# Kernel optimization log

Measured on AMD Instinct MI355X. Metric: run time of the kernel, lower is better.

## Reference

```python
import jax, jax.numpy as jnp
import numpy as np

C = 128
N = 4096
B = 4
NEG = -9e15


def _bn(x, g, b):
    # training-mode BatchNorm1d over (batch, N); x: [B, C, N]
    mean = x.mean(axis=(0, 2), keepdims=True)
    var = x.var(axis=(0, 2), keepdims=True)  # biased, like torch BN
    xh = (x - mean) * jax.lax.rsqrt(var + 1e-5)
    return xh * g[None, :, None] + b[None, :, None]


def _sa(x, mask2, wqk, wv, bv, wt, bt, g, b):
    # x: [B, C, N]; wqk: [C//4, C] (q and k share weights)
    xq = jnp.einsum('oc,bcn->bno', wqk, x)          # [B, N, C/4]
    xk = jnp.einsum('oc,bcm->bom', wqk, x)          # [B, C/4, N]
    energy = jnp.einsum('bno,bom->bnm', xq, xk)     # [B, N, N]
    energy = jnp.where(mask2, energy, NEG)
    attn = jax.nn.softmax(energy, axis=-1)
    # offset-attention: column-wise L1 renormalization
    attn = attn / (1e-9 + attn.sum(axis=1, keepdims=True))
    xv = jnp.einsum('oc,bcn->bon', wv, x) + bv[None, :, None]
    x_r = jnp.einsum('bcn,bnm->bcm', xv, attn)      # [B, C, N]
    x_r = jax.nn.relu(_bn(jnp.einsum('oc,bcn->bon', wt, x - x_r) + bt[None, :, None], g, b))
    return x + x_r


def setup_inputs() -> dict:
    key = jax.random.key(0)
    ks = jax.random.split(key, 12)
    s = 1.0 / np.sqrt(C)
    return {
        'x': jax.random.normal(ks[0], (B, C, N), jnp.float32),
        'mask': jax.random.randint(ks[1], (B, N), 0, 2, jnp.int32),
        'w1': jax.random.normal(ks[2], (C, C), jnp.float32) * s,
        'g1': jnp.ones((C,), jnp.float32),
        'b1': jnp.zeros((C,), jnp.float32),
        'w2': jax.random.normal(ks[3], (C, C), jnp.float32) * s,
        'g2': jnp.ones((C,), jnp.float32),
        'b2': jnp.zeros((C,), jnp.float32),
        'wqk': jax.random.normal(ks[4], (4, C // 4, C), jnp.float32) * s,
        'wv': jax.random.normal(ks[5], (4, C, C), jnp.float32) * s,
        'bv': jax.random.normal(ks[6], (4, C), jnp.float32) * 0.01,
        'wt': jax.random.normal(ks[7], (4, C, C), jnp.float32) * s,
        'bt': jax.random.normal(ks[8], (4, C), jnp.float32) * 0.01,
        'sg': jnp.ones((4, C), jnp.float32),
        'sb': jnp.zeros((4, C), jnp.float32),
    }


def reference(x, mask, w1, g1, b1, w2, g2, b2, wqk, wv, bv, wt, bt, sg, sb):
    m = mask.astype(bool)
    mask2 = m[:, :, None] & m[:, None, :]           # [B, N, N]
    x = jax.nn.relu(_bn(jnp.einsum('oc,bcn->bon', w1, x), g1, b1))
    x = jax.nn.relu(_bn(jnp.einsum('oc,bcn->bon', w2, x), g2, b2))
    outs = []
    h = x
    for i in range(4):
        h = _sa(h, mask2, wqk[i], wv[i], bv[i], wt[i], bt[i], sg[i], sb[i])
        outs.append(h)
    return jnp.concatenate(outs, axis=1)            # [B, 4C, N]
```

## Files before the change

### kernel.cpp

```cpp
#include <hip/hip_runtime.h>
#include <hip/hip_fp16.h>

constexpr int C = 128;
constexpr int N = 4096;
constexpr int B = 4;

typedef _Float16 f16x8 __attribute__((ext_vector_type(8)));
typedef _Float16 f16x4 __attribute__((ext_vector_type(4)));
typedef float    f32x4 __attribute__((ext_vector_type(4)));

__global__ __launch_bounds__(256) void k_wcvt(const float* __restrict__ w1,
                                              const float* __restrict__ w2,
                                              const float* __restrict__ wv,
                                              const float* __restrict__ wt,
                                              const float* __restrict__ wqk,
                                              _Float16* __restrict__ WF) {
  const int g = blockIdx.x * 256 + threadIdx.x;
  const float* src; int off;
  if (g < 4096)       { src = w1;  off = g; }
  else if (g < 8192)  { src = w2;  off = g - 4096; }
  else if (g < 24576) { src = wv;  off = g - 8192; }
  else if (g < 40960) { src = wt;  off = g - 24576; }
  else                { src = wqk; off = g - 40960; }
  const float4 v = ((const float4*)src)[off];
  f16x4 h = {(_Float16)v.x, (_Float16)v.y, (_Float16)v.z, (_Float16)v.w};
  *(f16x4*)&WF[(size_t)g * 4] = h;
}

__global__ __launch_bounds__(1024) void k_mask(const int* __restrict__ mask,
                                               int* __restrict__ psum,
                                               int* __restrict__ nvb) {
  const int b = blockIdx.x, tid = threadIdx.x;
  __shared__ int wsum[16];
  const int4 mv = *(const int4*)&mask[b * N + tid * 4];
  const int m0 = (mv.x != 0), m1 = (mv.y != 0), m2 = (mv.z != 0), m3 = (mv.w != 0);
  const int s0 = m0, s1 = s0 + m1, s2 = s1 + m2, s3 = s2 + m3;
  const int lane = tid & 63, w = tid >> 6;
  int sc = s3;
#pragma unroll
  for (int o = 1; o < 64; o <<= 1) {
    const int v = __shfl_up(sc, o, 64);
    if (lane >= o) sc += v;
  }
  if (lane == 63) wsum[w] = sc;
  __syncthreads();
  if (tid < 16) {
    int v = wsum[tid];
#pragma unroll
    for (int o = 1; o < 16; o <<= 1) {
      const int u = __shfl_up(v, o, 64);
      if (tid >= o) v += u;
    }
    wsum[tid] = v;
  }
  __syncthreads();
  const int excl = ((w > 0) ? wsum[w - 1] : 0) + sc - s3;
  int4 pv;
  pv.x = excl; pv.y = excl + s0; pv.z = excl + s1; pv.w = excl + s2;
  *(int4*)&psum[b * N + tid * 4] = pv;
  if (tid == 0) nvb[b] = wsum[15];
}

template<bool BIAS, bool STAT>
__global__ __launch_bounds__(512) void k_gwm(const _Float16* __restrict__ WF,
                                             const float* __restrict__ X,
                                             const float* __restrict__ bias,
                                             float* __restrict__ Y,
                                             float* __restrict__ bnpart) {
  __shared__ _Float16 XT[64 * 136];
  __shared__ float statP[4][64], statQ[4][64];
  const int tid = threadIdx.x;
  const int n0 = blockIdx.x * 64, oh = blockIdx.y, b = blockIdx.z;
  const float* Xb = X + (size_t)(b * C) * N + n0;
#pragma unroll
  for (int i = 0; i < 4; i++) {
    const int idx = tid + i * 512;
    const int c = idx >> 4, q = idx & 15;
    const float4 v = *(const float4*)&Xb[(size_t)c * N + q * 4];
    XT[(q * 4 + 0) * 136 + c] = (_Float16)v.x;
    XT[(q * 4 + 1) * 136 + c] = (_Float16)v.y;
    XT[(q * 4 + 2) * 136 + c] = (_Float16)v.z;
    XT[(q * 4 + 3) * 136 + c] = (_Float16)v.w;
  }
  __syncthreads();
  const int w = tid >> 6, lane = tid & 63, quad = lane >> 4, lr = lane & 15;
  const int nt = w & 3, og = w >> 2;
  const int ob[2] = {oh * 64 + og * 16, oh * 64 + (og + 2) * 16};
  f16x8 aW[2][4];
#pragma unroll
  for (int t = 0; t < 2; t++)
#pragma unroll
    for (int kc = 0; kc < 4; kc++)
      aW[t][kc] = *(const f16x8*)&WF[(size_t)(ob[t] + lr) * 128 + kc * 32 + quad * 8];
  f32x4 acc[2];
  acc[0] = (f32x4){0.f, 0.f, 0.f, 0.f};
  acc[1] = (f32x4){0.f, 0.f, 0.f, 0.f};
#pragma unroll
  for (int kc = 0; kc < 4; kc++) {
    const f16x8 bf = *(const f16x8*)&XT[(nt * 16 + lr) * 136 + kc * 32 + quad * 8];
    acc[0] = __builtin_amdgcn_mfma_f32_16x16x32_f16(aW[0][kc], bf, acc[0], 0, 0, 0);
    acc[1] = __builtin_amdgcn_mfma_f32_16x16x32_f16(aW[1][kc], bf, acc[1], 0, 0, 0);
  }
#pragma unroll
  for (int t = 0; t < 2; t++) {
#pragma unroll
    for (int r = 0; r < 4; r++) {
      const int o = ob[t] + quad * 4 + r;
      const float val = acc[t][r] + (BIAS ? bias[o] : 0.f);
      Y[(size_t)(b * C + o) * N + n0 + nt * 16 + lr] = val;
      if (STAT) {
        float s = val, q = val * val;
        s += __shfl_xor(s, 1, 64); q += __shfl_xor(q, 1, 64);
        s += __shfl_xor(s, 2, 64); q += __shfl_xor(q, 2, 64);
        s += __shfl_xor(s, 4, 64); q += __shfl_xor(q, 4, 64);
        s += __shfl_xor(s, 8, 64); q += __shfl_xor(q, 8, 64);
        if (lr == 0) { statP[nt][o - oh * 64] = s; statQ[nt][o - oh * 64] = q; }
      }
    }
  }
  if (STAT) {
    __syncthreads();
    if (tid < 64) {
      const int o = oh * 64 + tid;
      const float s = statP[0][tid] + statP[1][tid] + statP[2][tid] + statP[3][tid];
      const float q = statQ[0][tid] + statQ[1][tid] + statQ[2][tid] + statQ[3][tid];
      const int part = blockIdx.x * 4 + b;
      bnpart[o * 512 + part] = s;
      bnpart[o * 512 + 256 + part] = q;
    }
  }
}

__global__ __launch_bounds__(256) void k_qv(const _Float16* __restrict__ WFv,
                                            const _Float16* __restrict__ WFqk,
                                            const float* __restrict__ X,
                                            const float* __restrict__ bv,
                                            const int* __restrict__ mask,
                                            const int* __restrict__ psum,
                                            _Float16* __restrict__ XVc,
                                            _Float16* __restrict__ QT,
                                            _Float16* __restrict__ QTc,
                                            float* __restrict__ xvp) {
  __shared__ _Float16 XT[32 * 136];
  __shared__ float SP[2][128];
  const int tid = threadIdx.x;
  const int n0 = blockIdx.x * 32, b = blockIdx.y;
  const float* Xb = X + (size_t)(b * C) * N + n0;
#pragma unroll
  for (int i = 0; i < 4; i++) {
    const int idx = tid + i * 256;
    const int c = idx >> 3, q = idx & 7;
    const float4 v = *(const float4*)&Xb[(size_t)c * N + q * 4];
    XT[(q * 4 + 0) * 136 + c] = (_Float16)v.x;
    XT[(q * 4 + 1) * 136 + c] = (_Float16)v.y;
    XT[(q * 4 + 2) * 136 + c] = (_Float16)v.z;
    XT[(q * 4 + 3) * 136 + c] = (_Float16)v.w;
  }
  __syncthreads();
  const int w = tid >> 6, lane = tid & 63, quad = lane >> 4, lr = lane & 15;
  const int nt = w & 1, og = w >> 1;
  const int n = n0 + nt * 16 + lr;
  const int vld = mask[b * N + n] != 0;
  const int jc = psum[b * N + n];
  f32x4 acc[5];
  const _Float16* Aptr[5];
  int otl[5];
#pragma unroll
  for (int j = 0; j < 5; j++) {
    acc[j] = (f32x4){0.f, 0.f, 0.f, 0.f};
    const int ot = og + 2 * j;
    otl[j] = ot;
    Aptr[j] = (ot < 8) ? (WFv + (size_t)(ot * 16 + lr) * 128)
                       : (WFqk + (size_t)((ot - 8) * 16 + lr) * 128);
  }
#pragma unroll
  for (int kc = 0; kc < 4; kc++) {
    const f16x8 bf = *(const f16x8*)&XT[(nt * 16 + lr) * 136 + kc * 32 + quad * 8];
#pragma unroll
    for (int j = 0; j < 5; j++) {
      const f16x8 a = *(const f16x8*)&Aptr[j][kc * 32 + quad * 8];
      acc[j] = __builtin_amdgcn_mfma_f32_16x16x32_f16(a, bf, acc[j], 0, 0, 0);
    }
  }
#pragma unroll
  for (int j = 0; j < 5; j++) {
    const int ot = otl[j];
    if (ot < 8) {
      float v[4];
#pragma unroll
      for (int r = 0; r < 4; r++) v[r] = acc[j][r] + bv[ot * 16 + quad * 4 + r];
      if (vld) {
#pragma unroll
        for (int r = 0; r < 4; r++)
          XVc[(size_t)(b * C + ot * 16 + quad * 4 + r) * N + jc] = (_Float16)v[r];
      }
      float s[4];
#pragma unroll
      for (int r = 0; r < 4; r++) s[r] = vld ? 0.f : v[r];
#pragma unroll
      for (int o = 1; o <= 8; o <<= 1) {
#pragma unroll
        for (int r = 0; r < 4; r++) s[r] += __shfl_xor(s[r], o, 64);
      }
      if (lr == 0) {
#pragma unroll
        for (int r = 0; r < 4; r++) SP[nt][ot * 16 + quad * 4 + r] = s[r];
      }
    } else {
      f16x4 qv;
#pragma unroll
      for (int r = 0; r < 4; r++) qv[r] = (_Float16)acc[j][r];
      const int qo = (ot - 8) * 16 + quad * 4;
      *(f16x4*)&QT[((size_t)b * N + n) * 32 + qo] = qv;
      if (vld) *(f16x4*)&QTc[((size_t)b * N + jc) * 32 + qo] = qv;
    }
  }
  __syncthreads();
  if (tid < 128)
    xvp[(size_t)(b * C + tid) * 128 + blockIdx.x] = SP[0][tid] + SP[1][tid];
}

__global__ __launch_bounds__(64) void k_xvr(const float* __restrict__ xvp,
                                            float* __restrict__ xvi) {
  const int c = blockIdx.x, b = blockIdx.y, tid = threadIdx.x;
  const float* src = xvp + (size_t)(b * C + c) * 128;
  float v = src[tid] + src[tid + 64];
#pragma unroll
  for (int o = 1; o <= 32; o <<= 1) v += __shfl_xor(v, o, 64);
  if (tid == 0) xvi[b * C + c] = v;
}

__global__ __launch_bounds__(512) void k_sm(const _Float16* __restrict__ QTc,
                                            const int* __restrict__ nvb,
                                            float* __restrict__ rowmax,
                                            float* __restrict__ rowsi) {
  const int b = blockIdx.y;
  const int Nv = nvb[b];
  const int NvpB = (Nv + 63) & ~63;
  const int n0 = blockIdx.x * 64;
  if (n0 >= NvpB) return;
  __shared__ float mb[N];
  __shared__ float red[2][64];
  __shared__ float rmS[64];
  const int tid = threadIdx.x;
  const _Float16* Qb = QTc + (size_t)b * N * 32;
#pragma unroll
  for (int i = 0; i < 8; i++) {
    const int v = tid + i * 512;
    mb[v] = (v < Nv) ? 0.0f : -1e30f;
  }
  const int w = tid >> 6, lane = tid & 63, quad = lane >> 4, lr = lane & 15;
  const int nw = (w & 3) * 16, mh = (w >> 2) * 64;
  const f16x8 aF = *(const f16x8*)&Qb[(size_t)(n0 + nw + lr) * 32 + quad * 8];
  __syncthreads();
  float mx[4] = {-3e38f, -3e38f, -3e38f, -3e38f};
  for (int ms = 0; ms < NvpB; ms += 128) {
#pragma unroll
    for (int t = 0; t < 4; t++) {
      const int mrow = ms + mh + t * 16 + lr;
      const f16x8 bF = *(const f16x8*)&Qb[(size_t)mrow * 32 + quad * 8];
      f32x4 d = (f32x4){0.f, 0.f, 0.f, 0.f};
      d = __builtin_amdgcn_mfma_f32_16x16x32_f16(aF, bF, d, 0, 0, 0);
      const float bias = mb[mrow];
#pragma unroll
      for (int r = 0; r < 4; r++) mx[r] = fmaxf(mx[r], d[r] + bias);
    }
  }
#pragma unroll
  for (int r = 0; r < 4; r++) {
    float v = mx[r];
    v = fmaxf(v, __shfl_xor(v, 1, 64));
    v = fmaxf(v, __shfl_xor(v, 2, 64));
    v = fmaxf(v, __shfl_xor(v, 4, 64));
    v = fmaxf(v, __shfl_xor(v, 8, 64));
    mx[r] = v;
  }
  if (lr == 0)
#pragma unroll
    for (int r = 0; r < 4; r++) red[w >> 2][nw + quad * 4 + r] = mx[r];
  __syncthreads();
  if (tid < 64) rmS[tid] = fmaxf(red[0][tid], red[1][tid]);
  __syncthreads();
  float rmr[4];
#pragma unroll
  for (int r = 0; r < 4; r++) rmr[r] = rmS[nw + quad * 4 + r];
  float s[4] = {0.f, 0.f, 0.f, 0.f};
  for (int ms = 0; ms < NvpB; ms += 128) {
#pragma unroll
    for (int t = 0; t < 4; t++) {
      const int mrow = ms + mh + t * 16 + lr;
      const f16x8 bF = *(const f16x8*)&Qb[(size_t)mrow * 32 + quad * 8];
      f32x4 d = (f32x4){0.f, 0.f, 0.f, 0.f};
      d = __builtin_amdgcn_mfma_f32_16x16x32_f16(aF, bF, d, 0, 0, 0);
      const float bias = mb[mrow];
#pragma unroll
      for (int r = 0; r < 4; r++) s[r] += __expf(d[r] + bias - rmr[r]);
    }
  }
#pragma unroll
  for (int r = 0; r < 4; r++) {
    float v = s[r];
    v += __shfl_xor(v, 1, 64);
    v += __shfl_xor(v, 2, 64);
    v += __shfl_xor(v, 4, 64);
    v += __shfl_xor(v, 8, 64);
    s[r] = v;
  }
  __syncthreads();
  if (lr == 0)
#pragma unroll
    for (int r = 0; r < 4; r++) red[w >> 2][nw + quad * 4 + r] = s[r];
  __syncthreads();
  if (tid < 64) {
    const int row = n0 + tid;
    const float tot = red[0][tid] + red[1][tid];
    const bool valid = row < Nv;
    rowmax[b * N + row] = valid ? rmS[tid] : 1e30f;
    rowsi[b * N + row] = valid ? (1.0f / tot) : 0.0f;
  }
}

__global__ __launch_bounds__(512, 4) void k_pv(const _Float16* __restrict__ QT,
                                               const _Float16* __restrict__ QTc,
                                               const _Float16* __restrict__ XVc,
                                               const float* __restrict__ H,
                                               const int* __restrict__ mask,
                                               const float* __restrict__ rowmax,
                                               const float* __restrict__ rowsi,
                                               const int* __restrict__ nvb,
                                               const float* __restrict__ xvi,
                                               float* __restrict__ Td) {
  __shared__ _Float16 XVs[2][128 * 72];
  __shared__ _Float16 Ps[2][32 * 72];
  __shared__ float colPart[4][32];
  __shared__ float colS[32];
  const int tid = threadIdx.x;
  const int m0 = blockIdx.x * 32, b = blockIdx.y;
  const int Nv = nvb[b];
  const int ns = ((Nv + 63) & ~63) >> 6;
  const _Float16* Qa = QT + (size_t)b * N * 32;
  const _Float16* Qc = QTc + (size_t)b * N * 32;
  const _Float16* XVb = XVc + (size_t)(b * C) * N;
  const float* rmB = rowmax + b * N;
  const float* riB = rowsi + b * N;
  const int w = tid >> 6, lane = tid & 63, quad = lane >> 4, lr = lane & 15;
  const int msub = w & 1, nsub = w >> 1;
  const f16x8 aG = *(const f16x8*)&Qa[(size_t)(m0 + msub * 16 + lr) * 32 + quad * 8];
  float vmb[4];
#pragma unroll
  for (int r = 0; r < 4; r++)
    vmb[r] = (mask[b * N + m0 + msub * 16 + quad * 4 + r] != 0) ? 0.0f : -1e30f;
  const int sc0 = tid >> 3, sh0 = tid & 7;
  const int sc1 = sc0 + 64;
  f32x4 acc[2];
  acc[0] = (f32x4){0.f, 0.f, 0.f, 0.f};
  acc[1] = (f32x4){0.f, 0.f, 0.f, 0.f};
  float cs[4] = {0.f, 0.f, 0.f, 0.f};

  auto produce = [&](int k0, int bf) {
    const int nn = k0 + nsub * 16 + lr;
    const f16x8 bG = *(const f16x8*)&Qc[(size_t)nn * 32 + quad * 8];
    const f16x8 xv0 = *(const f16x8*)&XVb[(size_t)sc0 * N + k0 + sh0 * 8];
    const f16x8 xv1 = *(const f16x8*)&XVb[(size_t)sc1 * N + k0 + sh0 * 8];
    const float rmv = rmB[nn], riv = riB[nn];
    f32x4 e = (f32x4){0.f, 0.f, 0.f, 0.f};
    e = __builtin_amdgcn_mfma_f32_16x16x32_f16(aG, bG, e, 0, 0, 0);
    *(f16x8*)&XVs[bf][sc0 * 72 + sh0 * 8] = xv0;
    *(f16x8*)&XVs[bf][sc1 * 72 + sh0 * 8] = xv1;
#pragma unroll
    for (int r = 0; r < 4; r++) {
      const float p = __expf(e[r] - rmv + vmb[r]) * riv;
      cs[r] += p;
      Ps[bf][(msub * 16 + quad * 4 + r) * 72 + nsub * 16 + lr] = (_Float16)p;
    }
  };
  auto consume = [&](int bf) {
    const int c0 = w * 16;
    const f16x8 a0 = *(const f16x8*)&XVs[bf][(c0 + lr) * 72 + quad * 8];
    const f16x8 a1 = *(const f16x8*)&XVs[bf][(c0 + lr) * 72 + 32 + quad * 8];
    const f16x8 b00 = *(const f16x8*)&Ps[bf][lr * 72 + quad * 8];
    const f16x8 b01 = *(const f16x8*)&Ps[bf][lr * 72 + 32 + quad * 8];
    const f16x8 b10 = *(const f16x8*)&Ps[bf][(16 + lr) * 72 + quad * 8];
    const f16x8 b11 = *(const f16x8*)&Ps[bf][(16 + lr) * 72 + 32 + quad * 8];
    acc[0] = __builtin_amdgcn_mfma_f32_16x16x32_f16(a0, b00, acc[0], 0, 0, 0);
    acc[0] = __builtin_amdgcn_mfma_f32_16x16x32_f16(a1, b01, acc[0], 0, 0, 0);
    acc[1] = __builtin_amdgcn_mfma_f32_16x16x32_f16(a0, b10, acc[1], 0, 0, 0);
    acc[1] = __builtin_amdgcn_mfma_f32_16x16x32_f16(a1, b11, acc[1], 0, 0, 0);
  };

  if (ns > 0) produce(0, 0);
  __syncthreads();
  for (int it = 0; it < ns; it += 2) {
    if (it + 1 < ns) produce((it + 1) * 64, 1);
    consume(0);
    __syncthreads();
    if (it + 1 < ns) {
      if (it + 2 < ns) produce((it + 2) * 64, 0);
      consume(1);
      __syncthreads();
    }
  }
#pragma unroll
  for (int r = 0; r < 4; r++) {
    float v = cs[r];
    v += __shfl_xor(v, 1, 64);
    v += __shfl_xor(v, 2, 64);
    v += __shfl_xor(v, 4, 64);
    v += __shfl_xor(v, 8, 64);
    cs[r] = v;
  }
  if (lr == 0)
#pragma unroll
    for (int r = 0; r < 4; r++) colPart[nsub][msub * 16 + quad * 4 + r] = cs[r];
  __syncthreads();
  if (tid < 32)
    colS[tid] = colPart[0][tid] + colPart[1][tid] + colPart[2][tid] + colPart[3][tid];
  __syncthreads();
  const float ninvq = (float)(N - Nv) * 0.000244140625f;
  const float rdiv0 = 1.0f / (1e-9f + colS[lr] + ninvq);
  const float rdiv1 = 1.0f / (1e-9f + colS[16 + lr] + ninvq);
  const int cg = b * C + w * 16 + quad * 4;
#pragma unroll
  for (int r = 0; r < 4; r++) {
    const float xadd = xvi[cg + r] * 0.000244140625f;
    const size_t gi0 = (size_t)(cg + r) * N + m0 + lr;
    Td[gi0] = H[gi0] - (acc[0][r] + xadd) * rdiv0;
    const size_t gi1 = (size_t)(cg + r) * N + m0 + 16 + lr;
    Td[gi1] = H[gi1] - (acc[1][r] + xadd) * rdiv1;
  }
}

template<bool RES>
__global__ __launch_bounds__(256) void k_apply(const float* __restrict__ T2,
                                               const float* __restrict__ bnpart,
                                               const float* __restrict__ gamma,
                                               const float* __restrict__ beta,
                                               float* __restrict__ H,
                                               float* __restrict__ Out) {
  __shared__ float rs[4], rq[4], bc[2];
  const int tid = threadIdx.x;
  const int f = (blockIdx.x * 256 + tid) * 4;
  const int c = (blockIdx.x >> 2) & 127;
  float s = bnpart[c * 512 + tid];
  float q = bnpart[c * 512 + 256 + tid];
#pragma unroll
  for (int o = 1; o <= 32; o <<= 1) { s += __shfl_xor(s, o, 64); q += __shfl_xor(q, o, 64); }
  if ((tid & 63) == 0) { rs[tid >> 6] = s; rq[tid >> 6] = q; }
  __syncthreads();
  if (tid == 0) {
    const float st = rs[0] + rs[1] + rs[2] + rs[3];
    const float qt = rq[0] + rq[1] + rq[2] + rq[3];
    const float inv = 1.0f / (B * N);
    const float mean = st * inv;
    const float var = qt * inv - mean * mean;
    const float sc = gamma[c] * rsqrtf(var + 1e-5f);
    bc[0] = sc;
    bc[1] = beta[c] - mean * sc;
  }
  __syncthreads();
  const float sc = bc[0], sh = bc[1];
  const float4 t = *(const float4*)&T2[f];
  float4 r;
  r.x = fmaxf(t.x * sc + sh, 0.f);
  r.y = fmaxf(t.y * sc + sh, 0.f);
  r.z = fmaxf(t.z * sc + sh, 0.f);
  r.w = fmaxf(t.w * sc + sh, 0.f);
  if (RES) {
    const float4 h = *(const float4*)&H[f];
    r.x += h.x; r.y += h.y; r.z += h.z; r.w += h.w;
    *(float4*)&H[f] = r;
    const int b = f >> 19;
    const int rem = f & (C * N - 1);
    *(float4*)&Out[(size_t)b * (4 * C * N) + rem] = r;
  } else {
    *(float4*)&H[f] = r;
  }
}

extern "C" void kernel_launch(void* const* d_in, const int* in_sizes, int n_in,
                              void* d_out, int out_size, void* d_ws, size_t ws_size,
                              hipStream_t stream) {
  const float* x    = (const float*)d_in[0];
  const int*   mask = (const int*)  d_in[1];
  const float* w1   = (const float*)d_in[2];
  const float* g1   = (const float*)d_in[3];
  const float* b1   = (const float*)d_in[4];
  const float* w2   = (const float*)d_in[5];
  const float* g2   = (const float*)d_in[6];
  const float* b2   = (const float*)d_in[7];
  const float* wqk  = (const float*)d_in[8];
  const float* wv   = (const float*)d_in[9];
  const float* bv   = (const float*)d_in[10];
  const float* wt   = (const float*)d_in[11];
  const float* bt   = (const float*)d_in[12];
  const float* sg   = (const float*)d_in[13];
  const float* sb   = (const float*)d_in[14];
  float* out = (float*)d_out;

  char* p = (char*)d_ws;
  auto alloc = [&](size_t bytes) { char* r = p; p += (bytes + 255) & ~(size_t)255; return r; };
  float*    H      = (float*)   alloc((size_t)B * C * N * 4);
  float*    T2     = (float*)   alloc((size_t)B * C * N * 4);
  float*    Td     = (float*)   alloc((size_t)B * C * N * 4);
  _Float16* QT     = (_Float16*)alloc((size_t)B * N * 32 * 2);
  _Float16* QTc    = (_Float16*)alloc((size_t)B * N * 32 * 2);
  _Float16* XVc    = (_Float16*)alloc((size_t)B * C * N * 2);
  float*    rowmax = (float*)   alloc((size_t)B * N * 4);
  float*    rowsi  = (float*)   alloc((size_t)B * N * 4);
  float*    bnpart = (float*)   alloc((size_t)C * 512 * 4);
  int*      psum   = (int*)     alloc((size_t)B * N * 4);
  int*      nvb    = (int*)     alloc(256);
  float*    xvp    = (float*)   alloc((size_t)B * C * 128 * 4);
  float*    xvi    = (float*)   alloc((size_t)B * C * 4);
  _Float16* WF     = (_Float16*)alloc((size_t)180224 * 2);
  (void)ws_size;
  _Float16* wf1  = WF;
  _Float16* wf2  = WF + 16384;
  _Float16* wfv  = WF + 32768;
  _Float16* wft  = WF + 98304;
  _Float16* wfqk = WF + 163840;

  k_wcvt<<<176, 256, 0, stream>>>(w1, w2, wv, wt, wqk, WF);
  k_mask<<<B, 1024, 0, stream>>>(mask, psum, nvb);
  hipMemsetAsync(QTc, 0, (size_t)B * N * 32 * 2, stream);
  hipMemsetAsync(XVc, 0, (size_t)B * C * N * 2, stream);

  k_gwm<false, true><<<dim3(64, 2, B), 512, 0, stream>>>(wf1, x, nullptr, T2, bnpart);
  k_apply<false><<<2048, 256, 0, stream>>>(T2, bnpart, g1, b1, H, nullptr);
  k_gwm<false, true><<<dim3(64, 2, B), 512, 0, stream>>>(wf2, H, nullptr, T2, bnpart);
  k_apply<false><<<2048, 256, 0, stream>>>(T2, bnpart, g2, b2, H, nullptr);

  for (int L = 0; L < 4; L++) {
    k_qv<<<dim3(128, B), 256, 0, stream>>>(wfv + (size_t)L * 16384, wfqk + (size_t)L * 4096,
                                           H, bv + L * C, mask, psum, XVc, QT, QTc, xvp);
    k_xvr<<<dim3(C, B), 64, 0, stream>>>(xvp, xvi);
    k_sm<<<dim3(64, B), 512, 0, stream>>>(QTc, nvb, rowmax, rowsi);
    k_pv<<<dim3(128, B), 512, 0, stream>>>(QT, QTc, XVc, H, mask, rowmax, rowsi, nvb, xvi, Td);
    k_gwm<true, true><<<dim3(64, 2, B), 512, 0, stream>>>(wft + (size_t)L * 16384, Td, bt + L * C, T2, bnpart);
    k_apply<true><<<2048, 256, 0, stream>>>(T2, bnpart, sg + L * C, sb + L * C, H, out + (size_t)L * C * N);
  }
}
```

Measured before the change: 455.9 us.

## Tile XV layout for direct MFMA loads, single-pass online softmax stats

XV values are now stored in a tiled [channel-tile][key-block][16][64] layout, so k_pv can load MFMA A operands straight from global memory into registers. This removes the LDS staging buffer and its copies. k_sm switches from two passes (max, then sum of exp) to a single online-softmax pass that merges max and sum across lanes and waves, halving its QK MFMA work. Row max and inverse sum are packed into a float2 array, and the two memsets are merged into one, which relies on QTc and XVt being adjacent in the workspace. The online rescale adds extra exp calls and branches per element.

```diff
diff --git a/kernel.cpp b/kernel.cpp
--- a/kernel.cpp
+++ b/kernel.cpp
@@ -137,7 +137,7 @@
                                             const float* __restrict__ bv,
                                             const int* __restrict__ mask,
                                             const int* __restrict__ psum,
-                                            _Float16* __restrict__ XVc,
+                                            _Float16* __restrict__ XVt,
                                             _Float16* __restrict__ QT,
                                             _Float16* __restrict__ QTc,
                                             float* __restrict__ xvp) {
@@ -162,6 +162,7 @@
   const int n = n0 + nt * 16 + lr;
   const int vld = mask[b * N + n] != 0;
   const int jc = psum[b * N + n];
+  _Float16* XVb = XVt + (size_t)b * 524288;
   f32x4 acc[5];
   const _Float16* Aptr[5];
   int otl[5];
@@ -192,7 +193,8 @@
       if (vld) {
 #pragma unroll
         for (int r = 0; r < 4; r++)
-          XVc[(size_t)(b * C + ot * 16 + quad * 4 + r) * N + jc] = (_Float16)v[r];
+          XVb[((size_t)(ot * 64 + (jc >> 6)) * 16 + quad * 4 + r) * 64 + (jc & 63)] =
+              (_Float16)v[r];
       }
       float s[4];
 #pragma unroll
@@ -232,16 +234,14 @@
 
 __global__ __launch_bounds__(512) void k_sm(const _Float16* __restrict__ QTc,
                                             const int* __restrict__ nvb,
-                                            float* __restrict__ rowmax,
-                                            float* __restrict__ rowsi) {
+                                            float2* __restrict__ rowst) {
   const int b = blockIdx.y;
   const int Nv = nvb[b];
   const int NvpB = (Nv + 63) & ~63;
   const int n0 = blockIdx.x * 64;
   if (n0 >= NvpB) return;
   __shared__ float mb[N];
-  __shared__ float red[2][64];
-  __shared__ float rmS[64];
+  __shared__ float redM[2][64], redS[2][64];
   const int tid = threadIdx.x;
   const _Float16* Qb = QTc + (size_t)b * N * 32;
 #pragma unroll
@@ -254,6 +254,7 @@
   const f16x8 aF = *(const f16x8*)&Qb[(size_t)(n0 + nw + lr) * 32 + quad * 8];
   __syncthreads();
   float mx[4] = {-3e38f, -3e38f, -3e38f, -3e38f};
+  float s[4] = {0.f, 0.f, 0.f, 0.f};
   for (int ms = 0; ms < NvpB; ms += 128) {
 #pragma unroll
     for (int t = 0; t < 4; t++) {
@@ -263,74 +264,56 @@
       d = __builtin_amdgcn_mfma_f32_16x16x32_f16(aF, bF, d, 0, 0, 0);
       const float bias = mb[mrow];
 #pragma unroll
-      for (int r = 0; r < 4; r++) mx[r] = fmaxf(mx[r], d[r] + bias);
+      for (int r = 0; r < 4; r++) {
+        const float dv = d[r] + bias;
+        if (dv > mx[r]) {
+          s[r] *= __expf(mx[r] - dv);
+          mx[r] = dv;
+        }
+        s[r] += __expf(dv - mx[r]);
+      }
     }
   }
 #pragma unroll
   for (int r = 0; r < 4; r++) {
-    float v = mx[r];
-    v = fmaxf(v, __shfl_xor(v, 1, 64));
-    v = fmaxf(v, __shfl_xor(v, 2, 64));
-    v = fmaxf(v, __shfl_xor(v, 4, 64));
-    v = fmaxf(v, __shfl_xor(v, 8, 64));
-    mx[r] = v;
+#pragma unroll
+    for (int o = 1; o <= 8; o <<= 1) {
+      const float mo = __shfl_xor(mx[r], o, 64);
+      const float so = __shfl_xor(s[r], o, 64);
+      const float mn = fmaxf(mx[r], mo);
+      s[r] = s[r] * __expf(mx[r] - mn) + so * __expf(mo - mn);
+      mx[r] = mn;
+    }
   }
   if (lr == 0)
 #pragma unroll
-    for (int r = 0; r < 4; r++) red[w >> 2][nw + quad * 4 + r] = mx[r];
-  __syncthreads();
-  if (tid < 64) rmS[tid] = fmaxf(red[0][tid], red[1][tid]);
-  __syncthreads();
-  float rmr[4];
-#pragma unroll
-  for (int r = 0; r < 4; r++) rmr[r] = rmS[nw + quad * 4 + r];
-  float s[4] = {0.f, 0.f, 0.f, 0.f};
-  for (int ms = 0; ms < NvpB; ms += 128) {
-#pragma unroll
-    for (int t = 0; t < 4; t++) {
-      const int mrow = ms + mh + t * 16 + lr;
-      const f16x8 bF = *(const f16x8*)&Qb[(size_t)mrow * 32 + quad * 8];
-      f32x4 d = (f32x4){0.f, 0.f, 0.f, 0.f};
-      d = __builtin_amdgcn_mfma_f32_16x16x32_f16(aF, bF, d, 0, 0, 0);
-      const float bias = mb[mrow];
-#pragma unroll
-      for (int r = 0; r < 4; r++) s[r] += __expf(d[r] + bias - rmr[r]);
-    }
-  }
-#pragma unroll
-  for (int r = 0; r < 4; r++) {
-    float v = s[r];
-    v += __shfl_xor(v, 1, 64);
-    v += __shfl_xor(v, 2, 64);
-    v += __shfl_xor(v, 4, 64);
-    v += __shfl_xor(v, 8, 64);
-    s[r] = v;
-  }
-  __syncthreads();
-  if (lr == 0)
-#pragma unroll
-    for (int r = 0; r < 4; r++) red[w >> 2][nw + quad * 4 + r] = s[r];
+    for (int r = 0; r < 4; r++) {
+      redM[w >> 2][nw + quad * 4 + r] = mx[r];
+      redS[w >> 2][nw + quad * 4 + r] = s[r];
+    }
   __syncthreads();
   if (tid < 64) {
     const int row = n0 + tid;
-    const float tot = red[0][tid] + red[1][tid];
+    const float m0 = redM[0][tid], m1 = redM[1][tid];
+    const float M = fmaxf(m0, m1);
+    const float tot = redS[0][tid] * __expf(m0 - M) + redS[1][tid] * __expf(m1 - M);
     const bool valid = row < Nv;
-    rowmax[b * N + row] = valid ? rmS[tid] : 1e30f;
-    rowsi[b * N + row] = valid ? (1.0f / tot) : 0.0f;
+    float2 rv;
+    rv.x = valid ? M : 1e30f;
+    rv.y = valid ? (1.0f / tot) : 0.0f;
+    rowst[b * N + row] = rv;
   }
 }
 
 __global__ __launch_bounds__(512, 4) void k_pv(const _Float16* __restrict__ QT,
                                                const _Float16* __restrict__ QTc,
-                                               const _Float16* __restrict__ XVc,
+                                               const _Float16* __restrict__ XVt,
                                                const float* __restrict__ H,
                                                const int* __restrict__ mask,
-                                               const float* __restrict__ rowmax,
-                                               const float* __restrict__ rowsi,
+                                               const float2* __restrict__ rowst,
                                                const int* __restrict__ nvb,
                                                const float* __restrict__ xvi,
                                                float* __restrict__ Td) {
-  __shared__ _Float16 XVs[2][128 * 72];
   __shared__ _Float16 Ps[2][32 * 72];
   __shared__ float colPart[4][32];
   __shared__ float colS[32];
@@ -340,9 +323,8 @@
   const int ns = ((Nv + 63) & ~63) >> 6;
   const _Float16* Qa = QT + (size_t)b * N * 32;
   const _Float16* Qc = QTc + (size_t)b * N * 32;
-  const _Float16* XVb = XVc + (size_t)(b * C) * N;
-  const float* rmB = rowmax + b * N;
-  const float* riB = rowsi + b * N;
+  const _Float16* XVb = XVt + (size_t)b * 524288;
+  const float2* rsB = rowst + (size_t)b * N;
   const int w = tid >> 6, lane = tid & 63, quad = lane >> 4, lr = lane & 15;
   const int msub = w & 1, nsub = w >> 1;
   const f16x8 aG = *(const f16x8*)&Qa[(size_t)(m0 + msub * 16 + lr) * 32 + quad * 8];
@@ -350,34 +332,31 @@
 #pragma unroll
   for (int r = 0; r < 4; r++)
     vmb[r] = (mask[b * N + m0 + msub * 16 + quad * 4 + r] != 0) ? 0.0f : -1e30f;
-  const int sc0 = tid >> 3, sh0 = tid & 7;
-  const int sc1 = sc0 + 64;
   f32x4 acc[2];
   acc[0] = (f32x4){0.f, 0.f, 0.f, 0.f};
   acc[1] = (f32x4){0.f, 0.f, 0.f, 0.f};
   float cs[4] = {0.f, 0.f, 0.f, 0.f};
-
+  f16x8 aP0, aP1;
+
+  auto loadA = [&](int k0) {
+    const size_t base = ((size_t)(w * 64 + (k0 >> 6)) * 16 + lr) * 64 + quad * 8;
+    aP0 = *(const f16x8*)&XVb[base];
+    aP1 = *(const f16x8*)&XVb[base + 32];
+  };
   auto produce = [&](int k0, int bf) {
     const int nn = k0 + nsub * 16 + lr;
     const f16x8 bG = *(const f16x8*)&Qc[(size_t)nn * 32 + quad * 8];
-    const f16x8 xv0 = *(const f16x8*)&XVb[(size_t)sc0 * N + k0 + sh0 * 8];
-    const f16x8 xv1 = *(const f16x8*)&XVb[(size_t)sc1 * N + k0 + sh0 * 8];
-    const float rmv = rmB[nn], riv = riB[nn];
+    const float2 rr = rsB[nn];
     f32x4 e = (f32x4){0.f, 0.f, 0.f, 0.f};
     e = __builtin_amdgcn_mfma_f32_16x16x32_f16(aG, bG, e, 0, 0, 0);
-    *(f16x8*)&XVs[bf][sc0 * 72 + sh0 * 8] = xv0;
-    *(f16x8*)&XVs[bf][sc1 * 72 + sh0 * 8] = xv1;
 #pragma unroll
     for (int r = 0; r < 4; r++) {
-      const float p = __expf(e[r] - rmv + vmb[r]) * riv;
+      const float p = __expf(e[r] - rr.x + vmb[r]) * rr.y;
       cs[r] += p;
       Ps[bf][(msub * 16 + quad * 4 + r) * 72 + nsub * 16 + lr] = (_Float16)p;
     }
   };
-  auto consume = [&](int bf) {
-    const int c0 = w * 16;
-    const f16x8 a0 = *(const f16x8*)&XVs[bf][(c0 + lr) * 72 + quad * 8];
-    const f16x8 a1 = *(const f16x8*)&XVs[bf][(c0 + lr) * 72 + 32 + quad * 8];
+  auto consume = [&](int bf, f16x8 a0, f16x8 a1) {
     const f16x8 b00 = *(const f16x8*)&Ps[bf][lr * 72 + quad * 8];
     const f16x8 b01 = *(const f16x8*)&Ps[bf][lr * 72 + 32 + quad * 8];
     const f16x8 b10 = *(const f16x8*)&Ps[bf][(16 + lr) * 72 + quad * 8];
@@ -388,15 +367,17 @@
     acc[1] = __builtin_amdgcn_mfma_f32_16x16x32_f16(a1, b11, acc[1], 0, 0, 0);
   };
 
-  if (ns > 0) produce(0, 0);
+  if (ns > 0) { loadA(0); produce(0, 0); }
   __syncthreads();
   for (int it = 0; it < ns; it += 2) {
-    if (it + 1 < ns) produce((it + 1) * 64, 1);
-    consume(0);
+    const f16x8 a0c = aP0, a1c = aP1;
+    if (it + 1 < ns) { loadA((it + 1) * 64); produce((it + 1) * 64, 1); }
+    consume(0, a0c, a1c);
     __syncthreads();
     if (it + 1 < ns) {
-      if (it + 2 < ns) produce((it + 2) * 64, 0);
-      consume(1);
+      const f16x8 a0d = aP0, a1d = aP1;
+      if (it + 2 < ns) { loadA((it + 2) * 64); produce((it + 2) * 64, 0); }
+      consume(1, a0d, a1d);
       __syncthreads();
     }
   }
@@ -504,9 +485,8 @@
   float*    Td     = (float*)   alloc((size_t)B * C * N * 4);
   _Float16* QT     = (_Float16*)alloc((size_t)B * N * 32 * 2);
   _Float16* QTc    = (_Float16*)alloc((size_t)B * N * 32 * 2);
-  _Float16* XVc    = (_Float16*)alloc((size_t)B * C * N * 2);
-  float*    rowmax = (float*)   alloc((size_t)B * N * 4);
-  float*    rowsi  = (float*)   alloc((size_t)B * N * 4);
+  _Float16* XVt    = (_Float16*)alloc((size_t)B * 524288 * 2);
+  float2*   rowst  = (float2*)  alloc((size_t)B * N * 8);
   float*    bnpart = (float*)   alloc((size_t)C * 512 * 4);
   int*      psum   = (int*)     alloc((size_t)B * N * 4);
   int*      nvb    = (int*)     alloc(256);
@@ -522,8 +502,7 @@
 
   k_wcvt<<<176, 256, 0, stream>>>(w1, w2, wv, wt, wqk, WF);
   k_mask<<<B, 1024, 0, stream>>>(mask, psum, nvb);
-  hipMemsetAsync(QTc, 0, (size_t)B * N * 32 * 2, stream);
-  hipMemsetAsync(XVc, 0, (size_t)B * C * N * 2, stream);
+  hipMemsetAsync(QTc, 0, (size_t)B * N * 32 * 2 + (size_t)B * 524288 * 2, stream);
 
   k_gwm<false, true><<<dim3(64, 2, B), 512, 0, stream>>>(wf1, x, nullptr, T2, bnpart);
   k_apply<false><<<2048, 256, 0, stream>>>(T2, bnpart, g1, b1, H, nullptr);
@@ -532,10 +511,10 @@
 
   for (int L = 0; L < 4; L++) {
     k_qv<<<dim3(128, B), 256, 0, stream>>>(wfv + (size_t)L * 16384, wfqk + (size_t)L * 4096,
-                                           H, bv + L * C, mask, psum, XVc, QT, QTc, xvp);
+                                           H, bv + L * C, mask, psum, XVt, QT, QTc, xvp);
     k_xvr<<<dim3(C, B), 64, 0, stream>>>(xvp, xvi);
-    k_sm<<<dim3(64, B), 512, 0, stream>>>(QTc, nvb, rowmax, rowsi);
-    k_pv<<<dim3(128, B), 512, 0, stream>>>(QT, QTc, XVc, H, mask, rowmax, rowsi, nvb, xvi, Td);
+    k_sm<<<dim3(64, B), 512, 0, stream>>>(QTc, nvb, rowst);
+    k_pv<<<dim3(128, B), 512, 0, stream>>>(QT, QTc, XVt, H, mask, rowst, nvb, xvi, Td);
     k_gwm<true, true><<<dim3(64, 2, B), 512, 0, stream>>>(wft + (size_t)L * 16384, Td, bt + L * C, T2, bnpart);
     k_apply<true><<<2048, 256, 0, stream>>>(T2, bnpart, sg + L * C, sb + L * C, H, out + (size_t)L * C * N);
   }
```

New measurement: 519.4 us. 1.14x slower.
